# Performance work log

Measured on AMD Instinct MI355X. Metric: run time of the kernel, lower is better.

## Reference

```python
import jax, jax.numpy as jnp
import numpy as np
import math

EMBED_DIM = 1024
NUM_HEADS = 16
HEAD_DIM = EMBED_DIM // NUM_HEADS


def setup_inputs() -> dict:
    key = jax.random.key(0)
    ks = jax.random.split(key, 5)
    x = jax.random.normal(ks[0], (4, 2048, EMBED_DIM), dtype=jnp.float32)
    # Linear params (torch nn.Linear: y = x @ W.T + b); init scale ~ 1/sqrt(fan_in)
    s = 1.0 / math.sqrt(EMBED_DIM)
    qkv_w = jax.random.uniform(ks[1], (3 * EMBED_DIM, EMBED_DIM), jnp.float32, -s, s)
    qkv_b = jax.random.uniform(ks[2], (3 * EMBED_DIM,), jnp.float32, -s, s)
    proj_w = jax.random.uniform(ks[3], (EMBED_DIM, EMBED_DIM), jnp.float32, -s, s)
    proj_b = jax.random.uniform(ks[4], (EMBED_DIM,), jnp.float32, -s, s)
    return {"x": x, "qkv_w": qkv_w, "qkv_b": qkv_b, "proj_w": proj_w, "proj_b": proj_b}


def reference(x, qkv_w, qkv_b, proj_w, proj_b):
    bsz, num_tokens, dim = x.shape
    qkv = x @ qkv_w.T + qkv_b  # [B, S, 3*D]
    qkv = qkv.reshape(bsz, num_tokens, 3, NUM_HEADS, HEAD_DIM)
    qkv = jnp.transpose(qkv, (2, 0, 3, 1, 4))  # [3, B, H, S, hd]
    q, k, v = qkv[0], qkv[1], qkv[2]
    scale = 1.0 / math.sqrt(HEAD_DIM)
    attn_scores = jnp.einsum('bhqd,bhkd->bhqk', q, k) * scale  # [B, H, S, S]
    attn = jax.nn.softmax(attn_scores, axis=-1)
    out = jnp.einsum('bhqk,bhkd->bhqd', attn, v)  # [B, H, S, hd]
    out = jnp.transpose(out, (0, 2, 1, 3)).reshape(bsz, num_tokens, dim)
    out = out @ proj_w.T + proj_b
    return out
```

## Files before the change

### kernel.cpp

```cpp
#include <hip/hip_runtime.h>
#include <stdint.h>

#define DEVICE static __device__ __forceinline__

typedef __bf16 bf16x8 __attribute__((ext_vector_type(8)));
typedef float f32x4 __attribute__((ext_vector_type(4)));

#define AS1 __attribute__((address_space(1)))
#define AS3 __attribute__((address_space(3)))

DEVICE void g2l16(const void* gptr, void* lptr) {
  __builtin_amdgcn_global_load_lds((AS1 uint32_t*)(uintptr_t)gptr,
                                   (AS3 uint32_t*)(uint32_t)(uintptr_t)lptr,
                                   16, 0, 0);
}

DEVICE float b2f(ushort h) {
  union { uint32_t u; float f; } v;
  v.u = ((uint32_t)h) << 16;
  return v.f;
}
DEVICE ushort f2b(float f) {
  union { float f; uint32_t u; } v;
  v.f = f;
  uint32_t u = v.u;
  return (ushort)((u + 0x7FFFu + ((u >> 16) & 1u)) >> 16);
}

#if defined(__has_builtin) && __has_builtin(__builtin_amdgcn_exp2f)
DEVICE float fast_exp2(float x) { return __builtin_amdgcn_exp2f(x); }
#else
extern "C" __device__ float __ocml_native_exp2_f32(float);
DEVICE float fast_exp2(float x) { return __ocml_native_exp2_f32(x); }
#endif

#define QSCALE 0.1803368801111244f

DEVICE int kperm(int x) {
  return (x & 0x23) | ((x & 0x18) >> 1) | ((x & 0x4) << 2);
}

__global__ void detect_dtype(const ushort* __restrict__ xu, int* __restrict__ flag) {
  __shared__ int bad;
  if (threadIdx.x == 0) bad = 0;
  __syncthreads();
  int mybad = 0;
#pragma unroll
  for (int j = 0; j < 8; ++j) {
    const int i = threadIdx.x * 8 + j;
    const ushort u = xu[2 * i];
    const int e = (u >> 7) & 0xFF;
    if (!(e == 0 || (e >= 96 && e <= 160))) mybad++;
  }
  atomicAdd(&bad, mybad);
  __syncthreads();
  if (threadIdx.x == 0) *flag = (bad > 512) ? 1 : 0;
}

__global__ void convert_all(const void* __restrict__ s0, const void* __restrict__ s1,
                            const void* __restrict__ s2, const void* __restrict__ s3,
                            const void* __restrict__ s4,
                            ushort* __restrict__ d0, ushort* __restrict__ d1,
                            ushort* __restrict__ d2, ushort* __restrict__ d3,
                            ushort* __restrict__ d4,
                            const int* __restrict__ flag) {
  const bool isf32 = (*flag != 0);
  for (int g = blockIdx.x * blockDim.x + threadIdx.x; g < 1573376;
       g += gridDim.x * blockDim.x) {
    const void* src; ushort* dst; int i;
    if (g < 1048576)      { src = s0; dst = d0; i = g; }
    else if (g < 1441792) { src = s1; dst = d1; i = g - 1048576; }
    else if (g < 1442176) { src = s2; dst = d2; i = g - 1441792; }
    else if (g < 1573248) { src = s3; dst = d3; i = g - 1442176; }
    else                  { src = s4; dst = d4; i = g - 1573248; }
    ushort pk[8];
    if (isf32) {
      const float4 a = ((const float4*)src)[2 * i];
      const float4 b = ((const float4*)src)[2 * i + 1];
      pk[0] = f2b(a.x); pk[1] = f2b(a.y); pk[2] = f2b(a.z); pk[3] = f2b(a.w);
      pk[4] = f2b(b.x); pk[5] = f2b(b.y); pk[6] = f2b(b.z); pk[7] = f2b(b.w);
      *(uint4*)&dst[8 * i] = *(const uint4*)pk;
    } else {
      *(uint4*)&dst[8 * i] = ((const uint4*)src)[i];
    }
  }
}

template <int MODE, int GN>
__global__ __launch_bounds__(512, 2)
void gemm256(const ushort* __restrict__ A, const ushort* __restrict__ W,
             const ushort* __restrict__ bias, ushort* __restrict__ O0,
             ushort* __restrict__ O1, ushort* __restrict__ O2,
             int M, int N, int K, const int* __restrict__ flag)
{
  __shared__ __align__(16) char smem[131072];

  const int tid = threadIdx.x;
  const int lane = tid & 63;
  const int wave = tid >> 6;
  const int quad = lane >> 4;
  const int lo = lane & 15;
  const int swk = lo & 7;

  const int lin = blockIdx.y * gridDim.x + blockIdx.x;
  const int per = GN * gridDim.y;
  const int grp = lin / per;
  const int w   = lin % per;
  const int bxn = grp * GN + (w % GN);
  const int bym = w / GN;
  const int m0 = bym * 256;
  const int n0 = bxn * 256;

  const int wm = (wave >> 2) * 128;
  const int wn = (wave & 3) * 64;

  const int koffE = ((tid ^ (tid >> 3)) & 7) << 3;
  const int r0 = tid >> 3;
  const size_t offA = (size_t)(m0 + r0) * K + koffE;
  const size_t offB = (size_t)(n0 + r0) * K + koffE;
  const int NT = K >> 6;

  f32x4 acc[8][4] = {};

#pragma unroll
  for (int i = 0; i < 4; ++i) {
    g2l16(A + offA + (size_t)(64 * i) * K, smem + (wave << 10) + (i << 13));
    g2l16(W + offB + (size_t)(64 * i) * K, smem + 32768 + (wave << 10) + (i << 13));
  }
  asm volatile("s_waitcnt vmcnt(0)" ::: "memory");
  __builtin_amdgcn_s_barrier();

  for (int kt = 0; kt < NT; ++kt) {
    char* buf  = smem + (kt & 1) * 65536;
    char* nbuf = smem + ((kt + 1) & 1) * 65536;
    const ushort* Al = (const ushort*)buf;
    const ushort* Bl = (const ushort*)(buf + 32768);
    const bool pf = (kt + 1 < NT);
    const size_t nk = (size_t)(kt + 1) << 6;

    bf16x8 bfr[4][2];
#pragma unroll
    for (int p = 0; p < 4; ++p) {
      if (p == 0 && pf) {
#pragma unroll
        for (int i = 0; i < 4; ++i)
          g2l16(A + offA + (size_t)(64 * i) * K + nk,
                nbuf + (wave << 10) + (i << 13));
      }
      if (p == 1 && pf) {
#pragma unroll
        for (int i = 0; i < 4; ++i)
          g2l16(W + offB + (size_t)(64 * i) * K + nk,
                nbuf + 32768 + (wave << 10) + (i << 13));
      }
      if (p == 0) {
#pragma unroll
        for (int nt = 0; nt < 4; ++nt)
#pragma unroll
          for (int ks = 0; ks < 2; ++ks)
            bfr[nt][ks] = *(const bf16x8*)&Bl[(wn + nt * 16 + lo) * 64 +
                                              (((ks * 4 + quad) ^ swk) << 3)];
      }
      bf16x8 af[2][2];
#pragma unroll
      for (int mt2 = 0; mt2 < 2; ++mt2)
#pragma unroll
        for (int ks = 0; ks < 2; ++ks)
          af[mt2][ks] = *(const bf16x8*)&Al[(wm + (2 * p + mt2) * 16 + lo) * 64 +
                                            (((ks * 4 + quad) ^ swk) << 3)];
      __builtin_amdgcn_s_barrier();
      asm volatile("s_waitcnt lgkmcnt(0)" ::: "memory");
      __builtin_amdgcn_sched_barrier(0);
      __builtin_amdgcn_s_setprio(1);
#pragma unroll
      for (int mt2 = 0; mt2 < 2; ++mt2)
#pragma unroll
        for (int nt = 0; nt < 4; ++nt)
#pragma unroll
          for (int ks = 0; ks < 2; ++ks)
            acc[2 * p + mt2][nt] = __builtin_amdgcn_mfma_f32_16x16x32_bf16(
                af[mt2][ks], bfr[nt][ks], acc[2 * p + mt2][nt], 0, 0, 0);
      __builtin_amdgcn_s_setprio(0);
      __builtin_amdgcn_s_barrier();
    }
    if (pf) {
      asm volatile("s_waitcnt vmcnt(0)" ::: "memory");
      __builtin_amdgcn_s_barrier();
    }
  }

  if (MODE == 0) {
    const int which = n0 >> 10;
    if (which == 2) {
#pragma unroll
      for (int nt = 0; nt < 4; ++nt) {
        const int n = n0 + wn + nt * 16 + lo;
        const float bv = b2f(bias[n]);
        const int h = (n >> 6) & 15;
        const int d = n & 63;
#pragma unroll
        for (int mt = 0; mt < 8; ++mt) {
          const int m = m0 + wm + mt * 16 + quad * 4;
          const int b = m >> 11, s0 = m & 2047;
          ushort pk[4];
#pragma unroll
          for (int r = 0; r < 4; ++r) pk[r] = f2b(acc[mt][nt][r] + bv);
          *(uint2*)&O2[((size_t)(b * 16 + h) * 64 + d) * 2048 + s0] =
              *(const uint2*)pk;
        }
      }
    } else {
      const float qs = (which == 0) ? QSCALE : 1.0f;
      ushort* __restrict__ dst = (which == 0) ? O0 : O1;
      const int h = ((n0 + wn) >> 6) & 15;
      __syncthreads();
      ushort* scr = (ushort*)(smem + wave * 12288);
      float bv[4];
#pragma unroll
      for (int nt = 0; nt < 4; ++nt) bv[nt] = b2f(bias[n0 + wn + nt * 16 + lo]);
#pragma unroll
      for (int c2 = 0; c2 < 4; ++c2) {
#pragma unroll
        for (int mtl = 0; mtl < 2; ++mtl)
#pragma unroll
          for (int nt = 0; nt < 4; ++nt)
#pragma unroll
            for (int r = 0; r < 4; ++r)
              scr[(mtl * 16 + quad * 4 + r) * 88 + nt * 16 + lo] =
                  f2b((acc[c2 * 2 + mtl][nt][r] + bv[nt]) * qs);
        asm volatile("s_waitcnt lgkmcnt(0)" ::: "memory");
#pragma unroll
        for (int i = 0; i < 4; ++i) {
          const int id = lane + 64 * i;
          const int rowl = id >> 3, nch = id & 7;
          const uint4 val = *(const uint4*)&scr[rowl * 88 + nch * 8];
          const int m = m0 + wm + c2 * 32 + rowl;
          const int b = m >> 11;
          int s = m & 2047;
          if (which == 1) s = (s & ~63) | kperm(s & 63);
          *(uint4*)&dst[((size_t)(b * 16 + h) * 2048 + s) * 64 + nch * 8] = val;
        }
      }
    }
  } else {
    const bool f32out = (*flag != 0);
    float* Of = (float*)O0;
#pragma unroll
    for (int nt = 0; nt < 4; ++nt) {
      const int n = n0 + wn + nt * 16 + lo;
      const float bv = b2f(bias[n]);
#pragma unroll
      for (int mt = 0; mt < 8; ++mt)
#pragma unroll
        for (int r = 0; r < 4; ++r) {
          const int m = m0 + wm + mt * 16 + quad * 4 + r;
          const float val = acc[mt][nt][r] + bv;
          if (f32out) Of[(size_t)m * N + n] = val;
          else        O0[(size_t)m * N + n] = f2b(val);
        }
    }
  }
}

__global__ __launch_bounds__(256, 4)
void attn_fwd(const ushort* __restrict__ qp, const ushort* __restrict__ kp,
              const ushort* __restrict__ vp, ushort* __restrict__ o)
{
  __shared__ ushort Qs[128 * 64];
  __shared__ ushort Ks[64 * 64];
  __shared__ ushort Vt[64 * 64];

  const int tid = threadIdx.x;
  const int lane = tid & 63;
  const int wave = tid >> 6;
  const int quad = lane >> 4;
  const int lo = lane & 15;
  const int sw = (lo & 7) << 3;

  const int lin = blockIdx.y * gridDim.x + blockIdx.x;
  const int bh = (lin & 7) * 8 + ((lin >> 3) & 7);
  const int q0 = (lin >> 6) * 128;

  const ushort* Qg = qp + (size_t)bh * 2048 * 64;
  const ushort* Kg = kp + (size_t)bh * 2048 * 64;
  const ushort* Vg = vp + (size_t)bh * 64 * 2048;

#pragma unroll
  for (int i = 0; i < 4; ++i) {
    const int c = tid + 256 * i;
    const int row = c >> 3;
    const int kc = ((c ^ row) & 7) << 3;
    g2l16(Qg + (size_t)(q0 + row) * 64 + kc,
          (char*)Qs + ((wave << 6) + (i << 8)) * 16);
  }
  __syncthreads();

  bf16x8 qf[2][2];
#pragma unroll
  for (int mt = 0; mt < 2; ++mt)
#pragma unroll
    for (int ks = 0; ks < 2; ++ks)
      qf[mt][ks] = *(const bf16x8*)&Qs[(wave * 32 + mt * 16 + lo) * 64 +
                                       ((ks * 32 + quad * 8) ^ sw)];

  bf16x8 ones;
#pragma unroll
  for (int j = 0; j < 8; ++j) ones[j] = (__bf16)1.0f;

  f32x4 oacc[2][4] = {};
  f32x4 sumacc[2] = {};

  for (int j0 = 0; j0 < 2048; j0 += 64) {
    __syncthreads();
#pragma unroll
    for (int i = 0; i < 2; ++i) {
      const int c = tid + 256 * i;
      const int row = c >> 3;
      const int kc = ((c ^ row) & 7) << 3;
      g2l16(Kg + (size_t)(j0 + row) * 64 + kc,
            (char*)Ks + ((wave << 6) + (i << 8)) * 16);
      g2l16(Vg + (size_t)row * 2048 + j0 + kc,
            (char*)Vt + ((wave << 6) + (i << 8)) * 16);
    }
    __syncthreads();

    f32x4 sacc[2][4] = {};
#pragma unroll
    for (int ks = 0; ks < 2; ++ks) {
#pragma unroll
      for (int nt = 0; nt < 4; ++nt) {
        const bf16x8 kf =
            *(const bf16x8*)&Ks[(nt * 16 + lo) * 64 + ((ks * 32 + quad * 8) ^ sw)];
#pragma unroll
        for (int mt = 0; mt < 2; ++mt)
          sacc[mt][nt] = __builtin_amdgcn_mfma_f32_16x16x32_bf16(
              kf, qf[mt][ks], sacc[mt][nt], 0, 0, 0);
      }
    }

    bf16x8 pfr[2][2];
#pragma unroll
    for (int mt = 0; mt < 2; ++mt) {
      float p[4][4];
#pragma unroll
      for (int nt = 0; nt < 4; ++nt)
#pragma unroll
        for (int r = 0; r < 4; ++r)
          p[nt][r] = fast_exp2(sacc[mt][nt][r]);
#pragma unroll
      for (int b = 0; b < 2; ++b)
#pragma unroll
        for (int h = 0; h < 2; ++h)
#pragma unroll
          for (int r = 0; r < 4; ++r)
            pfr[mt][b][4 * h + r] = (__bf16)p[2 * b + h][r];
    }

#pragma unroll
    for (int b = 0; b < 2; ++b) {
#pragma unroll
      for (int mt = 0; mt < 2; ++mt)
        sumacc[mt] = __builtin_amdgcn_mfma_f32_16x16x32_bf16(
            pfr[mt][b], ones, sumacc[mt], 0, 0, 0);
#pragma unroll
      for (int dt = 0; dt < 4; ++dt) {
        const bf16x8 vf =
            *(const bf16x8*)&Vt[(dt * 16 + lo) * 64 + ((b * 32 + quad * 8) ^ sw)];
#pragma unroll
        for (int mt = 0; mt < 2; ++mt)
          oacc[mt][dt] = __builtin_amdgcn_mfma_f32_16x16x32_bf16(
              pfr[mt][b], vf, oacc[mt][dt], 0, 0, 0);
      }
    }
  }

  const int b_ = bh >> 4;
  const int h = bh & 15;
#pragma unroll
  for (int mt = 0; mt < 2; ++mt) {
#pragma unroll
    for (int r = 0; r < 4; ++r) {
      const float inv = 1.0f / sumacc[mt][r];
      const int srow = q0 + wave * 32 + mt * 16 + quad * 4 + r;
#pragma unroll
      for (int dt = 0; dt < 4; ++dt) {
        o[(((size_t)(b_ * 2048 + srow)) << 10) + h * 64 + dt * 16 + lo] =
            f2b(oacc[mt][dt][r] * inv);
      }
    }
  }
}

extern "C" void kernel_launch(void* const* d_in, const int* in_sizes, int n_in,
                              void* d_out, int out_size, void* d_ws, size_t ws_size,
                              hipStream_t stream) {
  const size_t N_X  = (size_t)4 * 2048 * 1024;
  const size_t N_WQ = (size_t)3072 * 1024;
  const size_t N_BQ = 3072;
  const size_t N_WP = (size_t)1024 * 1024;
  const size_t N_BP = 1024;
  const size_t HSD  = (size_t)64 * 2048 * 64;

  ushort* xb = (ushort*)d_ws;
  ushort* wq = xb + N_X;
  ushort* bq = wq + N_WQ;
  ushort* wp = bq + N_BQ;
  ushort* bp = wp + N_WP;
  ushort* qb = bp + N_BP;
  ushort* kb = qb + HSD;
  ushort* vb = kb + HSD;
  ushort* ab = vb + HSD;
  int* flag  = (int*)(ab + HSD);

  detect_dtype<<<1, 256, 0, stream>>>((const ushort*)d_in[0], flag);
  convert_all<<<2048, 256, 0, stream>>>(d_in[0], d_in[1], d_in[2], d_in[3], d_in[4],
                                        xb, wq, bq, wp, bp, flag);

  gemm256<0, 4><<<dim3(12, 32), dim3(512), 0, stream>>>(
      xb, wq, bq, qb, kb, vb, 8192, 3072, 1024, flag);
  attn_fwd<<<dim3(16, 64), dim3(256), 0, stream>>>(qb, kb, vb, ab);
  gemm256<1, 4><<<dim3(4, 32), dim3(512), 0, stream>>>(
      ab, wp, bp, (ushort*)d_out, nullptr, nullptr, 8192, 1024, 1024, flag);
}
```

Baseline: 268.7 us.

## Reorder A tile rows in LDS and pipeline loads with fine-grained vmcnt waits

Reorganizes the A tile layout in shared memory so that each compute phase p reads a contiguous 32-row chunk per wave group. The global-to-LDS prefetches are spread evenly across the four phases, and partial vmcnt waits replace the single full drain at the end of each k-step. This lets compute on early phases start once only their rows have arrived, overlapping load latency with MFMA work. The cost is fragile wait-count bookkeeping, where a wrong count could read stale LDS data.

Result: slower. 275.8 us (+2.6%).

```diff
diff --git a/kernel.cpp b/kernel.cpp
--- a/kernel.cpp
+++ b/kernel.cpp
@@ -101,6 +101,7 @@
   const int quad = lane >> 4;
   const int lo = lane & 15;
   const int swk = lo & 7;
+  const int wgm = wave >> 2;
 
   const int lin = blockIdx.y * gridDim.x + blockIdx.x;
   const int per = GN * gridDim.y;
@@ -111,47 +112,55 @@
   const int m0 = bym * 256;
   const int n0 = bxn * 256;
 
-  const int wm = (wave >> 2) * 128;
+  const int wm = wgm * 128;
   const int wn = (wave & 3) * 64;
 
   const int koffE = ((tid ^ (tid >> 3)) & 7) << 3;
-  const int r0 = tid >> 3;
-  const size_t offA = (size_t)(m0 + r0) * K + koffE;
-  const size_t offB = (size_t)(n0 + r0) * K + koffE;
+  const int rl = tid >> 3;
+  const int arow = m0 + (rl & 31) + ((rl >> 5) << 7);
+  const int brow = n0 + rl;
   const int NT = K >> 6;
 
   f32x4 acc[8][4] = {};
 
-#pragma unroll
-  for (int i = 0; i < 4; ++i) {
-    g2l16(A + offA + (size_t)(64 * i) * K, smem + (wave << 10) + (i << 13));
-    g2l16(W + offB + (size_t)(64 * i) * K, smem + 32768 + (wave << 10) + (i << 13));
-  }
-  asm volatile("s_waitcnt vmcnt(0)" ::: "memory");
+  {
+    char* nb = smem;
+    g2l16(A + (size_t)(arow +   0) * K + koffE, nb + tid * 16);
+    g2l16(W + (size_t)(brow +   0) * K + koffE, nb + 32768 + tid * 16);
+    g2l16(W + (size_t)(brow +  64) * K + koffE, nb + 40960 + tid * 16);
+    g2l16(W + (size_t)(brow + 128) * K + koffE, nb + 49152 + tid * 16);
+    g2l16(W + (size_t)(brow + 192) * K + koffE, nb + 57344 + tid * 16);
+    g2l16(A + (size_t)(arow +  32) * K + koffE, nb + 8192 + tid * 16);
+    g2l16(A + (size_t)(arow +  64) * K + koffE, nb + 16384 + tid * 16);
+    g2l16(A + (size_t)(arow +  96) * K + koffE, nb + 24576 + tid * 16);
+  }
+  asm volatile("s_waitcnt vmcnt(3)" ::: "memory");
   __builtin_amdgcn_s_barrier();
 
   for (int kt = 0; kt < NT; ++kt) {
-    char* buf  = smem + (kt & 1) * 65536;
-    char* nbuf = smem + ((kt + 1) & 1) * 65536;
-    const ushort* Al = (const ushort*)buf;
-    const ushort* Bl = (const ushort*)(buf + 32768);
+    const ushort* Al = (const ushort*)(smem + (kt & 1) * 65536);
+    const ushort* Bl = (const ushort*)(smem + (kt & 1) * 65536 + 32768);
+    char* nb = smem + ((kt + 1) & 1) * 65536;
     const bool pf = (kt + 1 < NT);
     const size_t nk = (size_t)(kt + 1) << 6;
 
     bf16x8 bfr[4][2];
 #pragma unroll
     for (int p = 0; p < 4; ++p) {
-      if (p == 0 && pf) {
-#pragma unroll
-        for (int i = 0; i < 4; ++i)
-          g2l16(A + offA + (size_t)(64 * i) * K + nk,
-                nbuf + (wave << 10) + (i << 13));
-      }
-      if (p == 1 && pf) {
-#pragma unroll
-        for (int i = 0; i < 4; ++i)
-          g2l16(W + offB + (size_t)(64 * i) * K + nk,
-                nbuf + 32768 + (wave << 10) + (i << 13));
+      if (pf) {
+        if (p == 0) {
+          g2l16(A + (size_t)(arow +   0) * K + nk + koffE, nb + tid * 16);
+          g2l16(W + (size_t)(brow +   0) * K + nk + koffE, nb + 32768 + tid * 16);
+        } else if (p == 1) {
+          g2l16(W + (size_t)(brow +  64) * K + nk + koffE, nb + 40960 + tid * 16);
+          g2l16(W + (size_t)(brow + 128) * K + nk + koffE, nb + 49152 + tid * 16);
+        } else if (p == 2) {
+          g2l16(W + (size_t)(brow + 192) * K + nk + koffE, nb + 57344 + tid * 16);
+          g2l16(A + (size_t)(arow +  32) * K + nk + koffE, nb + 8192 + tid * 16);
+        } else {
+          g2l16(A + (size_t)(arow +  64) * K + nk + koffE, nb + 16384 + tid * 16);
+          g2l16(A + (size_t)(arow +  96) * K + nk + koffE, nb + 24576 + tid * 16);
+        }
       }
       if (p == 0) {
 #pragma unroll
@@ -166,7 +175,8 @@
       for (int mt2 = 0; mt2 < 2; ++mt2)
 #pragma unroll
         for (int ks = 0; ks < 2; ++ks)
-          af[mt2][ks] = *(const bf16x8*)&Al[(wm + (2 * p + mt2) * 16 + lo) * 64 +
+          af[mt2][ks] = *(const bf16x8*)&Al[p * 4096 +
+                                            (wgm * 32 + mt2 * 16 + lo) * 64 +
                                             (((ks * 4 + quad) ^ swk) << 3)];
       __builtin_amdgcn_s_barrier();
       asm volatile("s_waitcnt lgkmcnt(0)" ::: "memory");
@@ -181,10 +191,16 @@
             acc[2 * p + mt2][nt] = __builtin_amdgcn_mfma_f32_16x16x32_bf16(
                 af[mt2][ks], bfr[nt][ks], acc[2 * p + mt2][nt], 0, 0, 0);
       __builtin_amdgcn_s_setprio(0);
-      __builtin_amdgcn_s_barrier();
-    }
-    if (pf) {
-      asm volatile("s_waitcnt vmcnt(0)" ::: "memory");
+      if (pf) {
+        if      (p == 0) asm volatile("s_waitcnt vmcnt(4)" ::: "memory");
+        else if (p == 1) asm volatile("s_waitcnt vmcnt(5)" ::: "memory");
+        else if (p == 2) asm volatile("s_waitcnt vmcnt(6)" ::: "memory");
+        else             asm volatile("s_waitcnt vmcnt(3)" ::: "memory");
+      } else {
+        if      (p == 0) asm volatile("s_waitcnt vmcnt(2)" ::: "memory");
+        else if (p == 1) asm volatile("s_waitcnt vmcnt(1)" ::: "memory");
+        else if (p == 2) asm volatile("s_waitcnt vmcnt(0)" ::: "memory");
+      }
       __builtin_amdgcn_s_barrier();
     }
   }
```
